# Optimization experiments

Hardware: AMD Instinct MI355X
Metric: run time of the kernel (lower is better)

Reference implementation:

```python
import jax, jax.numpy as jnp
import numpy as np

B, C, R = 1024, 256, 7          # batch, channels, ROI feature map res
PATCH, DIL = 16, 2              # correlation patch size, dilation_patch
REP = 1024                      # representation_size
FLAT = PATCH * PATCH * R * R    # 12544 = fc1 input dim


def setup_inputs() -> dict:
    key = jax.random.key(0)
    k = jax.random.split(key, 8)
    return {
        "patch1": jax.random.normal(k[0], (B, C, R, R), dtype=jnp.float32),
        "patch2": jax.random.normal(k[1], (B, C, R, R), dtype=jnp.float32),
        "W1": jax.random.normal(k[2], (REP, FLAT), dtype=jnp.float32) * 0.01,
        "b1": jnp.zeros((REP,), dtype=jnp.float32),
        "W2": jax.random.normal(k[3], (REP, REP), dtype=jnp.float32) * 0.02,
        "b2": jnp.zeros((REP,), dtype=jnp.float32),
        "W3": jax.random.normal(k[4], (4, REP), dtype=jnp.float32) * 0.02,
        "b3": jnp.zeros((4,), dtype=jnp.float32),
    }


def _correlate(p1, p2):
    """SpatialCorrelationSampler(patch_size=16, dilation_patch=2), kernel=1, stride=1.
    out[b, pi, pj, i, j] = sum_c p1[b,c,i,j] * p2[b,c, i+(pi-8)*2, j+(pj-8)*2]
    (zero outside bounds). Returns [B, PATCH*PATCH, R, R]."""
    pad = (PATCH // 2) * DIL  # 16; displacements span [-16, 14]
    p2p = jnp.pad(p2, ((0, 0), (0, 0), (pad, pad), (pad, pad)))  # [B,C,39,39]
    outs = []
    for pi in range(PATCH):
        for pj in range(PATCH):
            # shifted window: row offset (pi-8)*2 + pad = 2*pi, same for cols
            win = p2p[:, :, DIL * pi:DIL * pi + R, DIL * pj:DIL * pj + R]
            outs.append(jnp.einsum('bchw,bchw->bhw', p1, win))
    return jnp.stack(outs, axis=1)  # [B, 256, 7, 7] -> matches torch flatten order


def reference(patch1, patch2, W1, b1, W2, b2, W3, b3):
    x = _correlate(patch1, patch2).reshape(patch1.shape[0], -1)  # [B, 12544]
    x = jax.nn.relu(x @ W1.T + b1)
    x = jax.nn.relu(x @ W2.T + b2)
    pred_boxes = x @ W3.T + b3  # [B, 4]
    return pred_boxes
```

## Files before the change

### kernel.cpp

```cpp
#include <hip/hip_runtime.h>

#define BATCH 1024
#define RR    49
#define SP    12544
#define KVALID 625
#define KPAD   640
#define REP_N  1024

typedef __attribute__((ext_vector_type(4))) float f32x4;
typedef __attribute__((ext_vector_type(8))) short s16x8;

__device__ __forceinline__ unsigned short f2bf_rne(float f) {
    unsigned int u = __float_as_uint(f);
    unsigned int r = u + 0x7FFFu + ((u >> 16) & 1u);
    return (unsigned short)(r >> 16);
}
__device__ __forceinline__ float bf2f(unsigned short h) {
    return __uint_as_float(((unsigned int)h) << 16);
}
__device__ __forceinline__ void split2(float v, unsigned short& h, unsigned short& l) {
    h = f2bf_rne(v);
    l = f2bf_rne(v - bf2f(h));
}
__device__ __forceinline__ unsigned int cvtpk_bf16(float a, float b) {
    unsigned int r;
    asm("v_cvt_pk_bf16_f32 %0, %1, %2" : "=v"(r) : "v"(a), "v"(b));
    return r;
}
__device__ __forceinline__ void cvt8(const float* v, s16x8& hv, s16x8& lv) {
    unsigned int* hp = (unsigned int*)&hv;
    unsigned int* lp = (unsigned int*)&lv;
    #pragma unroll
    for (int i = 0; i < 4; ++i) {
        float v0 = v[2 * i], v1 = v[2 * i + 1];
        unsigned int ph = cvtpk_bf16(v0, v1);
        float h0 = __uint_as_float(ph << 16);
        float h1 = __uint_as_float(ph & 0xFFFF0000u);
        unsigned int pl = cvtpk_bf16(v0 - h0, v1 - h1);
        hp[i] = ph; lp[i] = pl;
    }
}

__device__ __forceinline__ void dec25(int u, int& i, int& d) {
    int ii = (u >= 4) + (u >= 7) + (u >= 11) + (u >= 14) + (u >= 18) + (u >= 21);
    int cum = (7 * ii + 1) >> 1;
    i = ii;
    d = 2 * (u - cum) + (ii & 1);
}
__device__ __forceinline__ int enc25(int i, int d) {
    return ((7 * i + 1) >> 1) + ((d - (i & 1)) >> 1);
}

__device__ __forceinline__ int kflat_of(int a) {
    int ar = a / 25, ac = a % 25;
    int i, dy, j, dx;
    dec25(ar, i, dy);
    dec25(ac, j, dx);
    int pi = (dy + 16 - i) >> 1;
    int pj = (dx + 16 - j) >> 1;
    return (pi * 16 + pj) * 49 + i * 7 + j;
}

#define MM(d, a, b) d = __builtin_amdgcn_mfma_f32_16x16x32_bf16(a, b, d, 0, 0, 0)

__global__ __launch_bounds__(256) void corr_prep_kernel(
    const float* __restrict__ p1, const float* __restrict__ p2,
    const float* __restrict__ W1, const float* __restrict__ W2,
    unsigned short* __restrict__ xh, unsigned short* __restrict__ xl,
    unsigned short* __restrict__ w1h, unsigned short* __restrict__ w1l,
    unsigned short* __restrict__ w2h, unsigned short* __restrict__ w2l)
{
    __shared__ float4 Tb[2][2][512];
    __shared__ unsigned short SXh[KPAD];
    __shared__ unsigned short SXl[KPAD];

    const int bid = blockIdx.x;
    const int t   = threadIdx.x;

    bool isCorr = false;
    int cid = 0, pid = 0;
    if (bid < 2048) {
        if ((bid & 1) == 0) { isCorr = true; cid = bid >> 1; }
        else                { pid = bid >> 1; }
    } else {
        pid = 1024 + (bid - 2048);
    }

    if (!isCorr) {
        if (pid < 2560) {
            int idx = pid * 256 + t;
            int n = idx / KPAD, a = idx - n * KPAD;
            float v = 0.f;
            if (a < KVALID) v = W1[(size_t)n * SP + kflat_of(a)];
            unsigned short h, l;
            split2(v, h, l);
            w1h[idx] = h; w1l[idx] = l;
        } else {
            int idx = ((pid - 2560) * 256 + t) * 4;
            float4 v = *(const float4*)&W2[idx];
            unsigned short h0, l0, h1, l1, h2, l2, h3, l3;
            split2(v.x, h0, l0); split2(v.y, h1, l1);
            split2(v.z, h2, l2); split2(v.w, h3, l3);
            *(ushort4*)&w2h[idx] = make_ushort4(h0, h1, h2, h3);
            *(ushort4*)&w2l[idx] = make_ushort4(l0, l1, l2, l3);
        }
        return;
    }

    const float* P1 = p1 + (size_t)cid * SP;
    const float* P2 = p2 + (size_t)cid * SP;

    const int wv   = t >> 6;
    const int lane = t & 63;
    const int fr   = lane & 15;
    const int fg   = (lane >> 4) * 8;

    const int ci = wv >> 1, cj = wv & 1;
    const int nj = 4 - cj;
    const int clsN = (4 - ci) * nj;
    const int pr = (fr < clsN) ? fr : 0;
    const int sPos = (2 * (pr / nj) + ci) * 7 + (2 * (pr % nj) + cj);

    const float* PS = (wv < 2) ? P1 : P2;
    const int tens  = wv >> 1;
    const int start = (wv & 1) * 4;

    #define STAGE(buf, hc)                                                     \
        do {                                                                   \
            const int off_ = (hc) * 1568;                                      \
            float4* T_ = &Tb[(buf)][tens][0];                                  \
            _Pragma("unroll")                                                  \
            for (int j_ = 0; j_ < 4; ++j_) {                                   \
                const int bq_  = start + j_;                                   \
                const int src_ = min(bq_ * 64 + lane, 391);                    \
                __builtin_amdgcn_global_load_lds(                              \
                    (const __attribute__((address_space(1))) unsigned int*)    \
                        (PS + off_ + src_ * 4),                                \
                    (__attribute__((address_space(3))) unsigned int*)          \
                        (T_ + bq_ * 64),                                       \
                    16, 0, 0);                                                 \
            }                                                                  \
        } while (0)

    for (int i = t; i < KPAD; i += 256) { SXh[i] = 0; SXl[i] = 0; }

    STAGE(0, 0);
    STAGE(1, 1);

    f32x4 acc = {};
    #pragma unroll
    for (int hc = 0; hc < 8; ++hc) {
        if (hc < 7) asm volatile("s_waitcnt vmcnt(4)" ::: "memory");
        else        asm volatile("s_waitcnt vmcnt(0)" ::: "memory");
        __builtin_amdgcn_s_barrier();
        __builtin_amdgcn_sched_barrier(0);

        const int cur = hc & 1;
        const float* Tf1 = (const float*)&Tb[cur][0][0];
        const float* Tf2 = (const float*)&Tb[cur][1][0];
        const int kb = fg * RR + sPos;
        float av[8], bv[8];
        #pragma unroll
        for (int i = 0; i < 8; ++i) {
            av[i] = Tf1[kb + i * RR];
            bv[i] = Tf2[kb + i * RR];
        }
        s16x8 ah, al, bh, bl;
        cvt8(av, ah, al);
        cvt8(bv, bh, bl);
        MM(acc, ah, bh);
        MM(acc, ah, bl);
        MM(acc, al, bh);

        __builtin_amdgcn_sched_barrier(0);
        __builtin_amdgcn_s_barrier();
        if (hc < 6) STAGE(cur, hc + 2);
    }
    #undef STAGE

    const int arow = (lane >> 4) * 4;
    if (fr < clsN) {
        const int dy = 2 * (fr / nj) + ci;
        const int dx = 2 * (fr % nj) + cj;
        #pragma unroll
        for (int r = 0; r < 4; ++r) {
            const int rowp = arow + r;
            if (rowp < clsN) {
                const int i1 = 2 * (rowp / nj) + ci;
                const int j1 = 2 * (rowp % nj) + cj;
                const int aidx = enc25(i1, dy) * 25 + enc25(j1, dx);
                unsigned short hh, ll;
                split2(acc[r], hh, ll);
                SXh[aidx] = hh; SXl[aidx] = ll;
            }
        }
    }
    __syncthreads();

    unsigned int* rh = (unsigned int*)(xh + (size_t)cid * KPAD);
    unsigned int* rl = (unsigned int*)(xl + (size_t)cid * KPAD);
    const unsigned int* sh = (const unsigned int*)SXh;
    const unsigned int* sl = (const unsigned int*)SXl;
    for (int i = t; i < KPAD / 2; i += 256) { rh[i] = sh[i]; rl[i] = sl[i]; }
}

template<bool SPLIT_OUT>
__global__ __launch_bounds__(256) void gemm_mfma(
    const unsigned short* __restrict__ Xh, const unsigned short* __restrict__ Xl, int ldx,
    const unsigned short* __restrict__ Wh, const unsigned short* __restrict__ Wl, int ldw,
    const float* __restrict__ bias, int K,
    float* __restrict__ Yf, unsigned short* __restrict__ Yh, unsigned short* __restrict__ Yl,
    int ldy)
{
    __shared__ unsigned short As[2][64][72];
    __shared__ unsigned short Bs[2][32][72];

    const int t = threadIdx.x;
    const int m_base = blockIdx.y * 64;
    const int n_base = blockIdx.x * 32;

    const int trow = t >> 2;
    const int tc   = (t & 3) * 8;
    const int trB  = t >> 3;
    const int tcB  = (t & 7) * 8;

    const unsigned short* xh_p = Xh + (size_t)(m_base + trow) * ldx + tc;
    const unsigned short* xl_p = Xl + (size_t)(m_base + trow) * ldx + tc;
    const unsigned short* wh_p = Wh + (size_t)(n_base + trB) * ldw + tcB;
    const unsigned short* wl_p = Wl + (size_t)(n_base + trB) * ldw + tcB;

    const int wv   = t >> 6;
    const int lane = t & 63;
    const int wr = (wv >> 1) * 32;
    const int wc = (wv & 1) * 16;
    const int fr = lane & 15;
    const int fg = (lane >> 4) * 8;

    f32x4 acc0 = {}, acc1 = {};

    for (int k0 = 0; k0 < K; k0 += 64) {
        s16x8 vxh0 = *(const s16x8*)(xh_p + k0);
        s16x8 vxh1 = *(const s16x8*)(xh_p + k0 + 32);
        s16x8 vxl0 = *(const s16x8*)(xl_p + k0);
        s16x8 vxl1 = *(const s16x8*)(xl_p + k0 + 32);
        s16x8 vwh  = *(const s16x8*)(wh_p + k0);
        s16x8 vwl  = *(const s16x8*)(wl_p + k0);
        __syncthreads();
        *(s16x8*)&As[0][trow][tc]      = vxh0;
        *(s16x8*)&As[0][trow][tc + 32] = vxh1;
        *(s16x8*)&As[1][trow][tc]      = vxl0;
        *(s16x8*)&As[1][trow][tc + 32] = vxl1;
        *(s16x8*)&Bs[0][trB][tcB]      = vwh;
        *(s16x8*)&Bs[1][trB][tcB]      = vwl;
        __syncthreads();

        #pragma unroll
        for (int ks = 0; ks < 2; ++ks) {
            const int ko = ks * 32 + fg;
            s16x8 ah0 = *(const s16x8*)&As[0][wr + fr][ko];
            s16x8 ah1 = *(const s16x8*)&As[0][wr + 16 + fr][ko];
            s16x8 al0 = *(const s16x8*)&As[1][wr + fr][ko];
            s16x8 al1 = *(const s16x8*)&As[1][wr + 16 + fr][ko];
            s16x8 bh  = *(const s16x8*)&Bs[0][wc + fr][ko];
            s16x8 bl  = *(const s16x8*)&Bs[1][wc + fr][ko];

            MM(acc0, ah0, bh); MM(acc0, ah0, bl); MM(acc0, al0, bh);
            MM(acc1, ah1, bh); MM(acc1, ah1, bl); MM(acc1, al1, bh);
        }
    }

    const int arow = (lane >> 4) * 4;
    const int col = n_base + wc + fr;
    const float bv = bias[col];
    #pragma unroll
    for (int mf = 0; mf < 2; ++mf) {
        const f32x4 a = mf == 0 ? acc0 : acc1;
        #pragma unroll
        for (int r = 0; r < 4; ++r) {
            const int row = m_base + wr + mf * 16 + arow + r;
            float v = fmaxf(a[r] + bv, 0.f);
            if (SPLIT_OUT) {
                unsigned short h, l;
                split2(v, h, l);
                Yh[(size_t)row * ldy + col] = h;
                Yl[(size_t)row * ldy + col] = l;
            } else {
                Yf[(size_t)row * ldy + col] = v;
            }
        }
    }
}

__global__ __launch_bounds__(256) void head_kernel(
    const float* __restrict__ h2, const float* __restrict__ W3,
    const float* __restrict__ b3, float* __restrict__ out)
{
    const int b = blockIdx.x;
    const int t = threadIdx.x;
    const float* row = h2 + (size_t)b * REP_N;

    float a0 = 0.f, a1 = 0.f, a2 = 0.f, a3 = 0.f;
    for (int k = t; k < REP_N; k += 256) {
        float x = row[k];
        a0 = fmaf(x, W3[k],             a0);
        a1 = fmaf(x, W3[REP_N + k],     a1);
        a2 = fmaf(x, W3[2 * REP_N + k], a2);
        a3 = fmaf(x, W3[3 * REP_N + k], a3);
    }
    #pragma unroll
    for (int off = 32; off > 0; off >>= 1) {
        a0 += __shfl_down(a0, off);
        a1 += __shfl_down(a1, off);
        a2 += __shfl_down(a2, off);
        a3 += __shfl_down(a3, off);
    }
    __shared__ float red[4][4];
    int wid = t >> 6, lane = t & 63;
    if (lane == 0) { red[wid][0] = a0; red[wid][1] = a1; red[wid][2] = a2; red[wid][3] = a3; }
    __syncthreads();
    if (t < 4) {
        out[b * 4 + t] = red[0][t] + red[1][t] + red[2][t] + red[3][t] + b3[t];
    }
}

extern "C" void kernel_launch(void* const* d_in, const int* in_sizes, int n_in,
                              void* d_out, int out_size, void* d_ws, size_t ws_size,
                              hipStream_t stream) {
    const float* p1 = (const float*)d_in[0];
    const float* p2 = (const float*)d_in[1];
    const float* W1 = (const float*)d_in[2];
    const float* b1 = (const float*)d_in[3];
    const float* W2 = (const float*)d_in[4];
    const float* b2 = (const float*)d_in[5];
    const float* W3 = (const float*)d_in[6];
    const float* b3 = (const float*)d_in[7];
    float* out = (float*)d_out;

    char* ws = (char*)d_ws;
    unsigned short* xh  = (unsigned short*)(ws + 0);
    unsigned short* xl  = (unsigned short*)(ws + 1310720);
    unsigned short* w1h = (unsigned short*)(ws + 2621440);
    unsigned short* w1l = (unsigned short*)(ws + 3932160);
    float*          h2  = (float*)(ws + 0);
    unsigned short* h1h = (unsigned short*)(ws + 5242880);
    unsigned short* h1l = (unsigned short*)(ws + 7340032);
    unsigned short* w2h = (unsigned short*)(ws + 9437184);
    unsigned short* w2l = (unsigned short*)(ws + 11534336);

    corr_prep_kernel<<<4608, 256, 0, stream>>>(
        p1, p2, W1, W2, xh, xl, w1h, w1l, w2h, w2l);

    gemm_mfma<true><<<dim3(32, 16), 256, 0, stream>>>(
        xh, xl, KPAD, w1h, w1l, KPAD, b1, KPAD,
        (float*)nullptr, h1h, h1l, REP_N);

    gemm_mfma<false><<<dim3(32, 16), 256, 0, stream>>>(
        h1h, h1l, REP_N, w2h, w2l, REP_N, b2, REP_N,
        h2, (unsigned short*)nullptr, (unsigned short*)nullptr, REP_N);

    head_kernel<<<BATCH, 256, 0, stream>>>(h2, W3, b3, out);
}
```

Baseline: 61.78 us.

## Process four batches per correlation block with a four-deep staging pipeline

Each correlation block now handles four consecutive batch items instead of one, and the shared-memory staging ring grows from two to four buffers so loads run three stages ahead and continue across batch boundaries. The grid shrinks from 4608 to 3840 blocks, and correlation blocks are interleaved one in every fifteen with the weight-conversion blocks. The aim is to amortize block launch and pipeline fill/drain cost and hide more global load latency. In exchange it doubles the staging LDS footprint, which may lower occupancy, and leaves fewer, longer correlation blocks, which can hurt load balance.

```diff
diff --git a/kernel.cpp b/kernel.cpp
--- a/kernel.cpp
+++ b/kernel.cpp
@@ -70,23 +70,16 @@
     unsigned short* __restrict__ w1h, unsigned short* __restrict__ w1l,
     unsigned short* __restrict__ w2h, unsigned short* __restrict__ w2l)
 {
-    __shared__ float4 Tb[2][2][512];
+    __shared__ float4 Tb[4][2][512];
     __shared__ unsigned short SXh[KPAD];
     __shared__ unsigned short SXl[KPAD];
 
     const int bid = blockIdx.x;
     const int t   = threadIdx.x;
 
-    bool isCorr = false;
-    int cid = 0, pid = 0;
-    if (bid < 2048) {
-        if ((bid & 1) == 0) { isCorr = true; cid = bid >> 1; }
-        else                { pid = bid >> 1; }
-    } else {
-        pid = 1024 + (bid - 2048);
-    }
-
+    const bool isCorr = (bid % 15) == 0;
     if (!isCorr) {
+        const int pid = bid - bid / 15 - 1;
         if (pid < 2560) {
             int idx = pid * 256 + t;
             int n = idx / KPAD, a = idx - n * KPAD;
@@ -107,8 +100,9 @@
         return;
     }
 
-    const float* P1 = p1 + (size_t)cid * SP;
-    const float* P2 = p2 + (size_t)cid * SP;
+    const int cid0 = (bid / 15) * 4;
+    const float* P1 = p1 + (size_t)cid0 * SP;
+    const float* P2 = p2 + (size_t)cid0 * SP;
 
     const int wv   = t >> 6;
     const int lane = t & 63;
@@ -125,9 +119,9 @@
     const int tens  = wv >> 1;
     const int start = (wv & 1) * 4;
 
-    #define STAGE(buf, hc)                                                     \
+    #define STAGE(buf, g)                                                      \
         do {                                                                   \
-            const int off_ = (hc) * 1568;                                      \
+            const int off_ = ((g) >> 3) * SP + ((g) & 7) * 1568;               \
             float4* T_ = &Tb[(buf)][tens][0];                                  \
             _Pragma("unroll")                                                  \
             for (int j_ = 0; j_ < 4; ++j_) {                                   \
@@ -142,66 +136,93 @@
             }                                                                  \
         } while (0)
 
+    #define PHASE(hc_, b4_, WAITN, DO_STAGE)                                   \
+        do {                                                                   \
+            asm volatile("s_waitcnt vmcnt(" #WAITN ")" ::: "memory");          \
+            __builtin_amdgcn_s_barrier();                                      \
+            __builtin_amdgcn_sched_barrier(0);                                 \
+            if (DO_STAGE) STAGE(((hc_) + 3) & 3, (b4_) * 8 + (hc_) + 3);       \
+            const float* Tf1 = (const float*)&Tb[(hc_) & 3][0][0];             \
+            const float* Tf2 = (const float*)&Tb[(hc_) & 3][1][0];             \
+            const int kb = fg * RR + sPos;                                     \
+            float av[8], bv[8];                                                \
+            _Pragma("unroll")                                                  \
+            for (int i_ = 0; i_ < 8; ++i_) {                                   \
+                av[i_] = Tf1[kb + i_ * RR];                                    \
+                bv[i_] = Tf2[kb + i_ * RR];                                    \
+            }                                                                  \
+            s16x8 ah, al, bh, bl;                                              \
+            cvt8(av, ah, al);                                                  \
+            cvt8(bv, bh, bl);                                                  \
+            MM(acc, ah, bh);                                                   \
+            MM(acc, ah, bl);                                                   \
+            MM(acc, al, bh);                                                   \
+            __builtin_amdgcn_sched_barrier(0);                                 \
+        } while (0)
+
+    #define EPI(bb_)                                                           \
+        do {                                                                   \
+            const int arow_ = (lane >> 4) * 4;                                 \
+            if (fr < clsN) {                                                   \
+                const int dy_ = 2 * (fr / nj) + ci;                            \
+                const int dx_ = 2 * (fr % nj) + cj;                            \
+                _Pragma("unroll")                                              \
+                for (int r_ = 0; r_ < 4; ++r_) {                               \
+                    const int rowp_ = arow_ + r_;                              \
+                    if (rowp_ < clsN) {                                        \
+                        const int i1_ = 2 * (rowp_ / nj) + ci;                 \
+                        const int j1_ = 2 * (rowp_ % nj) + cj;                 \
+                        const int ai_ = enc25(i1_, dy_) * 25 + enc25(j1_, dx_);\
+                        unsigned short hh_, ll_;                               \
+                        split2(acc[r_], hh_, ll_);                             \
+                        SXh[ai_] = hh_; SXl[ai_] = ll_;                        \
+                    }                                                          \
+                }                                                              \
+            }                                                                  \
+            asm volatile("s_waitcnt lgkmcnt(0)" ::: "memory");                 \
+            __builtin_amdgcn_sched_barrier(0);                                 \
+            __builtin_amdgcn_s_barrier();                                      \
+            unsigned int* rh_ = (unsigned int*)(xh + (size_t)(cid0+(bb_))*KPAD);\
+            unsigned int* rl_ = (unsigned int*)(xl + (size_t)(cid0+(bb_))*KPAD);\
+            const unsigned int* sh_ = (const unsigned int*)SXh;                \
+            const unsigned int* sl_ = (const unsigned int*)SXl;                \
+            for (int i_ = t; i_ < KPAD / 2; i_ += 256) {                       \
+                rh_[i_] = sh_[i_]; rl_[i_] = sl_[i_];                          \
+            }                                                                  \
+            acc = (f32x4){};                                                   \
+        } while (0)
+
     for (int i = t; i < KPAD; i += 256) { SXh[i] = 0; SXl[i] = 0; }
 
     STAGE(0, 0);
     STAGE(1, 1);
+    STAGE(2, 2);
 
     f32x4 acc = {};
-    #pragma unroll
-    for (int hc = 0; hc < 8; ++hc) {
-        if (hc < 7) asm volatile("s_waitcnt vmcnt(4)" ::: "memory");
-        else        asm volatile("s_waitcnt vmcnt(0)" ::: "memory");
-        __builtin_amdgcn_s_barrier();
-        __builtin_amdgcn_sched_barrier(0);
-
-        const int cur = hc & 1;
-        const float* Tf1 = (const float*)&Tb[cur][0][0];
-        const float* Tf2 = (const float*)&Tb[cur][1][0];
-        const int kb = fg * RR + sPos;
-        float av[8], bv[8];
-        #pragma unroll
-        for (int i = 0; i < 8; ++i) {
-            av[i] = Tf1[kb + i * RR];
-            bv[i] = Tf2[kb + i * RR];
-        }
-        s16x8 ah, al, bh, bl;
-        cvt8(av, ah, al);
-        cvt8(bv, bh, bl);
-        MM(acc, ah, bh);
-        MM(acc, ah, bl);
-        MM(acc, al, bh);
-
-        __builtin_amdgcn_sched_barrier(0);
-        __builtin_amdgcn_s_barrier();
-        if (hc < 6) STAGE(cur, hc + 2);
-    }
+    for (int b4 = 0; b4 < 3; ++b4) {
+        PHASE(0, b4, 8, true);
+        PHASE(1, b4, 8, true);
+        PHASE(2, b4, 8, true);
+        PHASE(3, b4, 8, true);
+        PHASE(4, b4, 8, true);
+        PHASE(5, b4, 8, true);
+        PHASE(6, b4, 8, true);
+        PHASE(7, b4, 8, true);
+        EPI(b4);
+    }
+    PHASE(0, 3, 8, true);
+    PHASE(1, 3, 8, true);
+    PHASE(2, 3, 8, true);
+    PHASE(3, 3, 8, true);
+    PHASE(4, 3, 8, true);
+    PHASE(5, 3, 8, false);
+    PHASE(6, 3, 4, false);
+    PHASE(7, 3, 0, false);
+    EPI(3);
+
     #undef STAGE
-
-    const int arow = (lane >> 4) * 4;
-    if (fr < clsN) {
-        const int dy = 2 * (fr / nj) + ci;
-        const int dx = 2 * (fr % nj) + cj;
-        #pragma unroll
-        for (int r = 0; r < 4; ++r) {
-            const int rowp = arow + r;
-            if (rowp < clsN) {
-                const int i1 = 2 * (rowp / nj) + ci;
-                const int j1 = 2 * (rowp % nj) + cj;
-                const int aidx = enc25(i1, dy) * 25 + enc25(j1, dx);
-                unsigned short hh, ll;
-                split2(acc[r], hh, ll);
-                SXh[aidx] = hh; SXl[aidx] = ll;
-            }
-        }
-    }
-    __syncthreads();
-
-    unsigned int* rh = (unsigned int*)(xh + (size_t)cid * KPAD);
-    unsigned int* rl = (unsigned int*)(xl + (size_t)cid * KPAD);
-    const unsigned int* sh = (const unsigned int*)SXh;
-    const unsigned int* sl = (const unsigned int*)SXl;
-    for (int i = t; i < KPAD / 2; i += 256) { rh[i] = sh[i]; rl[i] = sl[i]; }
+    #undef PHASE
+    #undef EPI
 }
 
 template<bool SPLIT_OUT>
@@ -347,7 +368,7 @@
     unsigned short* w2h = (unsigned short*)(ws + 9437184);
     unsigned short* w2l = (unsigned short*)(ws + 11534336);
 
-    corr_prep_kernel<<<4608, 256, 0, stream>>>(
+    corr_prep_kernel<<<3840, 256, 0, stream>>>(
         p1, p2, W1, W2, xh, xl, w1h, w1l, w2h, w2l);
 
     gemm_mfma<true><<<dim3(32, 16), 256, 0, stream>>>(
```

After: 67.46 us. 1.09x slower.

## Assign one batch item per wavefront in correlation kernel, dropping block barriers

Applied to the files above, without the earlier changes.

The correlation part of the prep kernel now gives each wavefront a whole batch item: it handles all four parity classes with four accumulators and has private LDS staging and output buffers. Block-level barriers are replaced by per-wave waitcnt, and the grid shrinks to 3840 blocks, with every 15th block doing correlation for four items. The aim is to remove cross-wave synchronisation and cut the number of correlation blocks. In exchange, each wave carries more registers, staging drops to single buffering with a full vmcnt(0) wait each chunk, and each block uses more LDS.

```diff
diff --git a/kernel.cpp b/kernel.cpp
--- a/kernel.cpp
+++ b/kernel.cpp
@@ -70,23 +70,15 @@
     unsigned short* __restrict__ w1h, unsigned short* __restrict__ w1l,
     unsigned short* __restrict__ w2h, unsigned short* __restrict__ w2l)
 {
-    __shared__ float4 Tb[2][2][512];
-    __shared__ unsigned short SXh[KPAD];
-    __shared__ unsigned short SXl[KPAD];
+    __shared__ float4 Tb[4][2][448];
+    __shared__ unsigned short SXh[4][KPAD];
+    __shared__ unsigned short SXl[4][KPAD];
 
     const int bid = blockIdx.x;
     const int t   = threadIdx.x;
 
-    bool isCorr = false;
-    int cid = 0, pid = 0;
-    if (bid < 2048) {
-        if ((bid & 1) == 0) { isCorr = true; cid = bid >> 1; }
-        else                { pid = bid >> 1; }
-    } else {
-        pid = 1024 + (bid - 2048);
-    }
-
-    if (!isCorr) {
+    if (bid % 15 != 0) {
+        const int pid = bid - bid / 15 - 1;
         if (pid < 2560) {
             int idx = pid * 256 + t;
             int n = idx / KPAD, a = idx - n * KPAD;
@@ -107,101 +99,120 @@
         return;
     }
 
+    const int wv   = t >> 6;
+    const int lane = t & 63;
+    const int cid  = (bid / 15) * 4 + wv;
     const float* P1 = p1 + (size_t)cid * SP;
     const float* P2 = p2 + (size_t)cid * SP;
 
-    const int wv   = t >> 6;
-    const int lane = t & 63;
-    const int fr   = lane & 15;
-    const int fg   = (lane >> 4) * 8;
-
-    const int ci = wv >> 1, cj = wv & 1;
-    const int nj = 4 - cj;
-    const int clsN = (4 - ci) * nj;
-    const int pr = (fr < clsN) ? fr : 0;
-    const int sPos = (2 * (pr / nj) + ci) * 7 + (2 * (pr % nj) + cj);
-
-    const float* PS = (wv < 2) ? P1 : P2;
-    const int tens  = wv >> 1;
-    const int start = (wv & 1) * 4;
-
-    #define STAGE(buf, hc)                                                     \
+    const int fr = lane & 15;
+    const int fg = (lane >> 4) * 8;
+
+    float4* T1 = &Tb[wv][0][0];
+    float4* T2 = &Tb[wv][1][0];
+    const float* Tf1 = (const float*)T1;
+    const float* Tf2 = (const float*)T2;
+
+    #define STAGE(cc)                                                          \
         do {                                                                   \
-            const int off_ = (hc) * 1568;                                      \
-            float4* T_ = &Tb[(buf)][tens][0];                                  \
+            const int off_ = (cc) * 1568;                                      \
             _Pragma("unroll")                                                  \
-            for (int j_ = 0; j_ < 4; ++j_) {                                   \
-                const int bq_  = start + j_;                                   \
-                const int src_ = min(bq_ * 64 + lane, 391);                    \
+            for (int j_ = 0; j_ < 7; ++j_) {                                   \
+                const int src_ = min(j_ * 64 + lane, 391);                     \
                 __builtin_amdgcn_global_load_lds(                              \
                     (const __attribute__((address_space(1))) unsigned int*)    \
-                        (PS + off_ + src_ * 4),                                \
+                        (P1 + off_ + src_ * 4),                                \
                     (__attribute__((address_space(3))) unsigned int*)          \
-                        (T_ + bq_ * 64),                                       \
+                        (T1 + j_ * 64),                                        \
+                    16, 0, 0);                                                 \
+            }                                                                  \
+            _Pragma("unroll")                                                  \
+            for (int j_ = 0; j_ < 7; ++j_) {                                   \
+                const int src_ = min(j_ * 64 + lane, 391);                     \
+                __builtin_amdgcn_global_load_lds(                              \
+                    (const __attribute__((address_space(1))) unsigned int*)    \
+                        (P2 + off_ + src_ * 4),                                \
+                    (__attribute__((address_space(3))) unsigned int*)          \
+                        (T2 + j_ * 64),                                        \
                     16, 0, 0);                                                 \
             }                                                                  \
         } while (0)
 
-    for (int i = t; i < KPAD; i += 256) { SXh[i] = 0; SXl[i] = 0; }
-
-    STAGE(0, 0);
-    STAGE(1, 1);
-
-    f32x4 acc = {};
+    STAGE(0);
+
+    for (int i = lane; i < KPAD; i += 64) { SXh[wv][i] = 0; SXl[wv][i] = 0; }
+
+    f32x4 acc0 = {}, acc1 = {}, acc2 = {}, acc3 = {};
+
+    for (int cc = 0; cc < 8; ++cc) {
+        asm volatile("s_waitcnt vmcnt(0)" ::: "memory");
+        __builtin_amdgcn_sched_barrier(0);
+
+        float av[4][8], bv[4][8];
+        #pragma unroll
+        for (int c = 0; c < 4; ++c) {
+            const int ci = c >> 1, cj = c & 1;
+            const int nj = 4 - cj;
+            const int clsN = (4 - ci) * nj;
+            const int pr = (fr < clsN) ? fr : 0;
+            const int sP = (2 * (pr / nj) + ci) * 7 + (2 * (pr % nj) + cj);
+            const int kb = fg * RR + sP;
+            #pragma unroll
+            for (int i = 0; i < 8; ++i) {
+                av[c][i] = Tf1[kb + i * RR];
+                bv[c][i] = Tf2[kb + i * RR];
+            }
+        }
+        asm volatile("s_waitcnt lgkmcnt(0)" ::: "memory");
+        __builtin_amdgcn_sched_barrier(0);
+        if (cc < 7) STAGE(cc + 1);
+
+        #pragma unroll
+        for (int c = 0; c < 4; ++c) {
+            s16x8 ah, al, bh, bl;
+            cvt8(av[c], ah, al);
+            cvt8(bv[c], bh, bl);
+            f32x4* ac = (c == 0) ? &acc0 : (c == 1) ? &acc1 : (c == 2) ? &acc2 : &acc3;
+            MM(*ac, ah, bh);
+            MM(*ac, ah, bl);
+            MM(*ac, al, bh);
+        }
+        __builtin_amdgcn_sched_barrier(0);
+    }
+    #undef STAGE
+
+    const int arow = (lane >> 4) * 4;
     #pragma unroll
-    for (int hc = 0; hc < 8; ++hc) {
-        if (hc < 7) asm volatile("s_waitcnt vmcnt(4)" ::: "memory");
-        else        asm volatile("s_waitcnt vmcnt(0)" ::: "memory");
-        __builtin_amdgcn_s_barrier();
-        __builtin_amdgcn_sched_barrier(0);
-
-        const int cur = hc & 1;
-        const float* Tf1 = (const float*)&Tb[cur][0][0];
-        const float* Tf2 = (const float*)&Tb[cur][1][0];
-        const int kb = fg * RR + sPos;
-        float av[8], bv[8];
-        #pragma unroll
-        for (int i = 0; i < 8; ++i) {
-            av[i] = Tf1[kb + i * RR];
-            bv[i] = Tf2[kb + i * RR];
-        }
-        s16x8 ah, al, bh, bl;
-        cvt8(av, ah, al);
-        cvt8(bv, bh, bl);
-        MM(acc, ah, bh);
-        MM(acc, ah, bl);
-        MM(acc, al, bh);
-
-        __builtin_amdgcn_sched_barrier(0);
-        __builtin_amdgcn_s_barrier();
-        if (hc < 6) STAGE(cur, hc + 2);
-    }
-    #undef STAGE
-
-    const int arow = (lane >> 4) * 4;
-    if (fr < clsN) {
-        const int dy = 2 * (fr / nj) + ci;
-        const int dx = 2 * (fr % nj) + cj;
-        #pragma unroll
-        for (int r = 0; r < 4; ++r) {
-            const int rowp = arow + r;
-            if (rowp < clsN) {
-                const int i1 = 2 * (rowp / nj) + ci;
-                const int j1 = 2 * (rowp % nj) + cj;
-                const int aidx = enc25(i1, dy) * 25 + enc25(j1, dx);
-                unsigned short hh, ll;
-                split2(acc[r], hh, ll);
-                SXh[aidx] = hh; SXl[aidx] = ll;
+    for (int c = 0; c < 4; ++c) {
+        const int ci = c >> 1, cj = c & 1;
+        const int nj = 4 - cj;
+        const int clsN = (4 - ci) * nj;
+        const f32x4 a = (c == 0) ? acc0 : (c == 1) ? acc1 : (c == 2) ? acc2 : acc3;
+        if (fr < clsN) {
+            const int dy = 2 * (fr / nj) + ci;
+            const int dx = 2 * (fr % nj) + cj;
+            #pragma unroll
+            for (int r = 0; r < 4; ++r) {
+                const int rowp = arow + r;
+                if (rowp < clsN) {
+                    const int i1 = 2 * (rowp / nj) + ci;
+                    const int j1 = 2 * (rowp % nj) + cj;
+                    const int aidx = enc25(i1, dy) * 25 + enc25(j1, dx);
+                    unsigned short hh, ll;
+                    split2(a[r], hh, ll);
+                    SXh[wv][aidx] = hh; SXl[wv][aidx] = ll;
+                }
             }
         }
     }
-    __syncthreads();
+    asm volatile("s_waitcnt lgkmcnt(0)" ::: "memory");
+    __builtin_amdgcn_sched_barrier(0);
 
     unsigned int* rh = (unsigned int*)(xh + (size_t)cid * KPAD);
     unsigned int* rl = (unsigned int*)(xl + (size_t)cid * KPAD);
-    const unsigned int* sh = (const unsigned int*)SXh;
-    const unsigned int* sl = (const unsigned int*)SXl;
-    for (int i = t; i < KPAD / 2; i += 256) { rh[i] = sh[i]; rl[i] = sl[i]; }
+    const unsigned int* sh = (const unsigned int*)&SXh[wv][0];
+    const unsigned int* sl = (const unsigned int*)&SXl[wv][0];
+    for (int i = lane; i < KPAD / 2; i += 64) { rh[i] = sh[i]; rl[i] = sl[i]; }
 }
 
 template<bool SPLIT_OUT>
@@ -347,7 +358,7 @@
     unsigned short* w2h = (unsigned short*)(ws + 9437184);
     unsigned short* w2l = (unsigned short*)(ws + 11534336);
 
-    corr_prep_kernel<<<4608, 256, 0, stream>>>(
+    corr_prep_kernel<<<3840, 256, 0, stream>>>(
         p1, p2, W1, W2, xh, xl, w1h, w1l, w2h, w2l);
 
     gemm_mfma<true><<<dim3(32, 16), 256, 0, stream>>>(
```

Result: no change. 61.42 us (-0.6%).
